# Kernel tuning notes

Hardware: AMD Instinct MI355X
Metric: run time of the kernel (lower is better)

Reference implementation:

```python
import jax, jax.numpy as jnp
import numpy as np

DIM = 192
HEADS = 4
EMBED = 48


def setup_inputs() -> dict:
    key = jax.random.key(0)
    ks = jax.random.split(key, 8)
    b, c, h, w = 8, DIM, 128, 128
    x = jax.random.normal(ks[0], (b, c, h, w), dtype=jnp.float32)
    prior = jax.random.normal(ks[1], (b, 1, EMBED * 4), dtype=jnp.float32)
    # learned params (bias=False)
    w_qkv = jax.random.normal(ks[2], (3 * c, c), dtype=jnp.float32) * (1.0 / np.sqrt(c))
    w_dw = jax.random.normal(ks[3], (3 * c, 1, 3, 3), dtype=jnp.float32) * (1.0 / 3.0)
    w_proj = jax.random.normal(ks[4], (c, c), dtype=jnp.float32) * (1.0 / np.sqrt(c))
    w_kernel = jax.random.normal(ks[5], (2 * c, EMBED * 4), dtype=jnp.float32) * (1.0 / np.sqrt(EMBED * 4))
    temperature = jnp.ones((HEADS, 1, 1), dtype=jnp.float32)
    return {"x": x, "prior": prior, "w_qkv": w_qkv, "w_dw": w_dw,
            "w_proj": w_proj, "w_kernel": w_kernel, "temperature": temperature}


def _mdta(x, prior, w_qkv, w_dw, w_proj, w_kernel, temperature):
    b, c, h, w = x.shape
    # prior modulation: Linear(4*embed -> 2*dim), broadcast over (h,w)
    kv = jnp.einsum('blf,of->blo', prior, w_kernel)[:, 0]        # (b, 2c)
    kv1, kv2 = kv[:, :c], kv[:, c:]
    x = x * kv1[:, :, None, None] + kv2[:, :, None, None]
    # 1x1 conv -> depthwise 3x3 conv
    qkv = jnp.einsum('bchw,oc->bohw', x, w_qkv)                   # (b, 3c, h, w)
    qkv = jax.lax.conv_general_dilated(
        qkv, w_dw, window_strides=(1, 1), padding='SAME',
        dimension_numbers=('NCHW', 'OIHW', 'NCHW'), feature_group_count=3 * c)
    q, k, v = jnp.split(qkv, 3, axis=1)
    ch = c // HEADS
    def heads(t):  # (b, c, h, w) -> (b, head, ch, h*w)
        return t.reshape(b, HEADS, ch, h * w)
    q, k, v = heads(q), heads(k), heads(v)
    # L2 normalize over the (h w) reduction axis
    q = q / jnp.linalg.norm(q, axis=-1, keepdims=True).clip(1e-12)
    k = k / jnp.linalg.norm(k, axis=-1, keepdims=True).clip(1e-12)
    attn = jnp.einsum('bhcn,bhdn->bhcd', q, k) * temperature      # (b, head, ch, ch)
    attn = jax.nn.softmax(attn, axis=-1)
    out = jnp.einsum('bhcd,bhdn->bhcn', attn, v).reshape(b, c, h, w)
    return jnp.einsum('bchw,oc->bohw', out, w_proj)


def reference(x, prior, w_qkv, w_dw, w_proj, w_kernel, temperature):
    return _mdta(x, prior, w_qkv, w_dw, w_proj, w_kernel, temperature)
```

## Files before the change

kernel.cpp:

```cpp
#include <hip/hip_runtime.h>
#include <hip/hip_bf16.h>
#include <stdint.h>

typedef float f32x4 __attribute__((ext_vector_type(4)));
typedef __bf16 bf16x8 __attribute__((ext_vector_type(8)));
typedef __bf16 bf16x4 __attribute__((ext_vector_type(4)));
typedef __bf16 bf16x2 __attribute__((ext_vector_type(2)));

#define NB 8
#define NC 192
#define NO 576
#define NH 128
#define NWID 128
#define NSP 16384
#define NHEADS 4
#define NCH 48

#define OFF_KV    0u
#define OFF_SSQ   12288u
#define OFF_S     24576u
#define OFF_WB    319488u
#define OFF_M     540672u
#define OFF_XT    1130496u
#define OFF_QKV1  152125440u

#define GR(r) (((r) ^ ((r) >> 2)) & 7)

__device__ __forceinline__ void g2l16(const void* g, void* l) {
    __builtin_amdgcn_global_load_lds((const __attribute__((address_space(1))) void*)g,
                                     (__attribute__((address_space(3))) void*)l, 16, 0, 0);
}

__global__ void k_prep(const float* __restrict__ prior, const float* __restrict__ w_kernel,
                       const float* __restrict__ w_qkv, float* __restrict__ kv,
                       float* __restrict__ zbase, __bf16* __restrict__ Wb) {
    int t = blockIdx.x * 256 + threadIdx.x;
    if (t < 76800) zbase[t] = 0.f;
    if (t < NO * NC) Wb[t] = (__bf16)w_qkv[t];
    if (t < NB * 384) {
        int b = t / 384, j = t % 384;
        const float* p = prior + b * NC;
        const float* wk = w_kernel + j * NC;
        float s = 0.f;
        for (int f = 0; f < NC; ++f) s += p[f] * wk[f];
        kv[t] = s;
    }
}

__global__ __launch_bounds__(256) void k_xt(const float* __restrict__ x, const float* __restrict__ kv,
                                            __bf16* __restrict__ xt) {
    int b = blockIdx.y;
    int n0 = blockIdx.x * 128;
    __shared__ __align__(16) __bf16 lds[128 * 192];
    int t = threadIdx.x;
    for (int p = 0; p < 24; ++p) {
        int id = p * 256 + t;
        int c = id >> 5, n4 = (id & 31) << 2;
        f32x4 v = *reinterpret_cast<const f32x4*>(x + (size_t)(b * NC + c) * NSP + n0 + n4);
        float k1 = kv[b * 384 + c], k2 = kv[b * 384 + 192 + c];
        int chi = (c >> 3) ^ ((n4 >> 2) & 7);
        int base = chi * 16 + (c & 7) * 2;
#pragma unroll
        for (int j = 0; j < 4; ++j)
            *reinterpret_cast<__bf16*>((char*)lds + (n4 + j) * 384 + base) = (__bf16)(v[j] * k1 + k2);
    }
    __syncthreads();
    for (int p = 0; p < 12; ++p) {
        int id = p * 256 + t;
        int n = id / 24, k = id % 24;
        bf16x8 r = *reinterpret_cast<const bf16x8*>((char*)lds + n * 384 + ((k ^ ((n >> 2) & 7)) << 4));
        *reinterpret_cast<bf16x8*>(xt + (size_t)(b * NSP + n0 + n) * NC + k * 8) = r;
    }
}

__global__ __launch_bounds__(256, 3) void k_qkv(const __bf16* __restrict__ xt, const __bf16* __restrict__ Wb,
                                                __bf16* __restrict__ qkv1) {
    __shared__ __align__(16) char lds[49152];
    int b = blockIdx.y, n0 = blockIdx.x * 64;
    int t = threadIdx.x;
    const __bf16* bsrc = xt + (size_t)(b * NSP + n0) * NC;
#pragma unroll
    for (int i = 0; i < 6; ++i) {
        int s = i * 256 + t;
        int r = s / 24, c = s % 24, g = c ^ (r & 7);
        g2l16(bsrc + (size_t)r * NC + g * 8, lds + s * 16);
    }
#pragma unroll
    for (int i = 0; i < 6; ++i) {
        int s = i * 256 + t;
        int r = s / 24, c = s % 24, g = c ^ (r & 7);
        g2l16(Wb + (size_t)r * NC + g * 8, lds + 24576 + s * 16);
    }
    asm volatile("s_waitcnt vmcnt(0)" ::: "memory");
    __syncthreads();
    int w = t >> 6, l = t & 63, lr = l & 15, lg = l >> 4;
    bf16x8 bgf[6];
#pragma unroll
    for (int ks = 0; ks < 6; ++ks) {
        int c16 = ks * 4 + lg;
        int r = w * 16 + lr;
        bgf[ks] = *reinterpret_cast<const bf16x8*>(lds + r * 384 + ((c16 ^ (r & 7)) << 4));
    }
    for (int ot = 0; ot < 9; ++ot) {
        f32x4 acc[4] = {};
#pragma unroll
        for (int ks = 0; ks < 6; ++ks) {
            int c16 = ks * 4 + lg;
            bf16x8 a[4];
#pragma unroll
            for (int mf = 0; mf < 4; ++mf) {
                int r = mf * 16 + lr;
                a[mf] = *reinterpret_cast<const bf16x8*>(lds + 24576 + r * 384 + ((c16 ^ (r & 7)) << 4));
            }
#pragma unroll
            for (int mf = 0; mf < 4; ++mf)
                acc[mf] = __builtin_amdgcn_mfma_f32_16x16x32_bf16(a[mf], bgf[ks], acc[mf], 0, 0, 0);
        }
        __syncthreads();
        if (ot < 8) {
            const __bf16* asrc = Wb + (size_t)(ot + 1) * 64 * NC;
#pragma unroll
            for (int i = 0; i < 6; ++i) {
                int s = i * 256 + t;
                int r = s / 24, c = s % 24, g = c ^ (r & 7);
                g2l16(asrc + (size_t)r * NC + g * 8, lds + 24576 + s * 16);
            }
            __builtin_amdgcn_sched_barrier(0);
        }
        int o0 = ot * 64;
#pragma unroll
        for (int mf = 0; mf < 4; ++mf)
#pragma unroll
            for (int rr = 0; rr < 4; ++rr) {
                int orow = o0 + mf * 16 + lg * 4 + rr;
                qkv1[(size_t)(b * NO + orow) * NSP + n0 + w * 16 + lr] = (__bf16)acc[mf][rr];
            }
        if (ot < 8) {
            asm volatile("s_waitcnt vmcnt(16)" ::: "memory");
            __syncthreads();
        }
    }
}

__global__ __launch_bounds__(256) void k_dw(const __bf16* __restrict__ qkv1, const float* __restrict__ w_dw,
                                            __bf16* __restrict__ qkv2, float* __restrict__ ssq) {
    int task = blockIdx.x * 4 + (threadIdx.x >> 6);
    int l = threadIdx.x & 63;
    int strip = task & 7;
    int bo = task >> 3;
    int o = bo % NO, b = bo / NO;
    const __bf16* src = qkv1 + (size_t)bo * NSP;
    __bf16* dst = qkv2 + (size_t)bo * NSP;
    float wd[9];
#pragma unroll
    for (int i = 0; i < 9; ++i) wd[i] = w_dw[o * 9 + i];
    int ys = strip * 16;
    float a0, b0, L0, R0, a1, b1, L1, R1, a2, b2, L2, R2;

#define LOADROW(Y, A, B, L_, R_) {                                            \
        bf16x2 p = {};                                                        \
        int y_ = (Y);                                                         \
        if (y_ >= 0 && y_ < NH) p = *reinterpret_cast<const bf16x2*>(src + y_ * NWID + 2 * l); \
        A = (float)p[0]; B = (float)p[1];                                     \
        L_ = __shfl(B, l - 1); R_ = __shfl(A, l + 1);                         \
        if (l == 0) L_ = 0.f;                                                 \
        if (l == 63) R_ = 0.f; }

    LOADROW(ys - 1, a0, b0, L0, R0)
    LOADROW(ys,     a1, b1, L1, R1)
    float ss = 0.f;
    bool qk = (o < 384);
#pragma unroll 4
    for (int i = 0; i < 16; ++i) {
        LOADROW(ys + i + 1, a2, b2, L2, R2)
        float oa = L0 * wd[0] + a0 * wd[1] + b0 * wd[2]
                 + L1 * wd[3] + a1 * wd[4] + b1 * wd[5]
                 + L2 * wd[6] + a2 * wd[7] + b2 * wd[8];
        float ob = a0 * wd[0] + b0 * wd[1] + R0 * wd[2]
                 + a1 * wd[3] + b1 * wd[4] + R1 * wd[5]
                 + a2 * wd[6] + b2 * wd[7] + R2 * wd[8];
        bf16x2 ov; ov[0] = (__bf16)oa; ov[1] = (__bf16)ob;
        *reinterpret_cast<bf16x2*>(dst + (ys + i) * NWID + 2 * l) = ov;
        if (qk) { float fa = (float)ov[0], fb = (float)ov[1]; ss += fa * fa + fb * fb; }
        a0 = a1; b0 = b1; L0 = L1; R0 = R1;
        a1 = a2; b1 = b2; L1 = L2; R1 = R2;
    }
#undef LOADROW
    if (qk) {
        for (int off = 32; off > 0; off >>= 1) ss += __shfl_down(ss, off);
        if (l == 0) atomicAdd(&ssq[b * 384 + o], ss);
    }
}

__global__ __launch_bounds__(256, 3) void k_sdot(const __bf16* __restrict__ qkv2, float* __restrict__ S) {
    __shared__ __align__(16) char lds[49152];
    int b = blockIdx.z, h = blockIdx.y, n0 = blockIdx.x * 512;
    int t = threadIdx.x;
    int w = t >> 6, l = t & 63, lr = l & 15, lg = l >> 4;
    const __bf16* qsrc = qkv2 + (size_t)(b * NO + h * NCH) * NSP + n0;
    const __bf16* ksrc = qkv2 + (size_t)(b * NO + 192 + h * NCH) * NSP + n0;
    f32x4 acc[3][3] = {};
    for (int pass = 0; pass < 2; ++pass) {
        if (pass) __syncthreads();
        int coff = pass * 256;
#pragma unroll
        for (int i = 0; i < 6; ++i) {
            int s = i * 256 + t;
            int r = s >> 5, c = s & 31, g = c ^ (r & 7);
            g2l16(qsrc + (size_t)r * NSP + coff + g * 8, lds + s * 16);
        }
#pragma unroll
        for (int i = 0; i < 6; ++i) {
            int s = i * 256 + t;
            int r = s >> 5, c = s & 31, g = c ^ (r & 7);
            g2l16(ksrc + (size_t)r * NSP + coff + g * 8, lds + 24576 + s * 16);
        }
        asm volatile("s_waitcnt vmcnt(0)" ::: "memory");
        __syncthreads();
#pragma unroll
        for (int j = 0; j < 2; ++j) {
            int c16 = (w * 2 + j) * 4 + lg;
            bf16x8 a[3], bb[3];
#pragma unroll
            for (int mf = 0; mf < 3; ++mf) {
                int r = mf * 16 + lr;
                a[mf] = *reinterpret_cast<const bf16x8*>(lds + r * 512 + ((c16 ^ (r & 7)) << 4));
            }
#pragma unroll
            for (int nf = 0; nf < 3; ++nf) {
                int r = nf * 16 + lr;
                bb[nf] = *reinterpret_cast<const bf16x8*>(lds + 24576 + r * 512 + ((c16 ^ (r & 7)) << 4));
            }
#pragma unroll
            for (int mf = 0; mf < 3; ++mf)
#pragma unroll
                for (int nf = 0; nf < 3; ++nf)
                    acc[mf][nf] = __builtin_amdgcn_mfma_f32_16x16x32_bf16(a[mf], bb[nf], acc[mf][nf], 0, 0, 0);
        }
    }
    __syncthreads();
    float* red = (float*)lds;
#pragma unroll
    for (int mf = 0; mf < 3; ++mf)
#pragma unroll
        for (int nf = 0; nf < 3; ++nf)
#pragma unroll
            for (int r = 0; r < 4; ++r) {
                int c = mf * 16 + lg * 4 + r, d = nf * 16 + lr;
                red[(w * 48 + c) * 49 + d] = acc[mf][nf][r];
            }
    __syncthreads();
    float* Sb = S + (size_t)(b * NHEADS + h) * NCH * NCH;
    for (int i = 0; i < 9; ++i) {
        int idx = t + i * 256;
        int c = idx / 48, d = idx % 48;
        float s = red[c * 49 + d] + red[(48 + c) * 49 + d] + red[(96 + c) * 49 + d] + red[(144 + c) * 49 + d];
        atomicAdd(&Sb[c * 48 + d], s);
    }
}

__global__ __launch_bounds__(256) void k_soft(const float* __restrict__ S, const float* __restrict__ ssq,
                                              const float* __restrict__ temp, const float* __restrict__ w_proj,
                                              __bf16* __restrict__ M) {
    int b = blockIdx.x / NHEADS, h = blockIdx.x % NHEADS;
    int tid = threadIdx.x;
    __shared__ float attn[48][48];
    __shared__ float inv[96];
    if (tid < 96) {
        int c = tid % 48;
        int isK = tid / 48;
        float v = ssq[b * 384 + isK * 192 + h * NCH + c];
        float nrm = fmaxf(sqrtf(v), 1e-12f);
        inv[tid] = 1.f / nrm;
    }
    __syncthreads();
    float tp = temp[h];
    const float* Sb = S + (size_t)(b * NHEADS + h) * NCH * NCH;
    for (int i = 0; i < 9; ++i) {
        int idx = tid + i * 256;
        int c = idx / 48, d = idx % 48;
        attn[c][d] = Sb[c * 48 + d] * inv[c] * inv[48 + d] * tp;
    }
    __syncthreads();
    if (tid < 48) {
        float m = -1e30f;
        for (int d = 0; d < 48; ++d) m = fmaxf(m, attn[tid][d]);
        float sum = 0.f;
        for (int d = 0; d < 48; ++d) { float e = __expf(attn[tid][d] - m); attn[tid][d] = e; sum += e; }
        float r = 1.f / sum;
        for (int d = 0; d < 48; ++d) attn[tid][d] *= r;
    }
    __syncthreads();
    for (int i = 0; i < 36; ++i) {
        int idx = tid + i * 256;
        int oo = idx / 48, d = idx % 48;
        const float* wp = w_proj + oo * NC + h * NCH;
        float s = 0.f;
        for (int c = 0; c < 48; ++c) s += wp[c] * attn[c][d];
        M[(size_t)(b * NC + oo) * NC + h * NCH + d] = (__bf16)s;
    }
}

__global__ __launch_bounds__(256, 2) void k_out(const __bf16* __restrict__ Mw, const __bf16* __restrict__ qkv2,
                                                float* __restrict__ outp) {
    __shared__ __align__(16) char lds[73728];
    int b = blockIdx.y, n0 = blockIdx.x * 128;
    int t = threadIdx.x;
    const __bf16* asrc0 = Mw + (size_t)(b * NC) * NC;
#pragma unroll
    for (int i = 0; i < 6; ++i) {
        int s = i * 256 + t;
        int r = s / 24, c = s % 24, g = c ^ GR(r);
        g2l16(asrc0 + (size_t)r * NC + g * 8, lds + 49152 + s * 16);
    }
    const __bf16* vb = qkv2 + (size_t)(b * NO + 384) * NSP + n0;
#pragma unroll 4
    for (int p = 0; p < 24; ++p) {
        int id = p * 256 + t;
        int c = id >> 5, n4 = (id & 31) << 2;
        bf16x4 vv = *reinterpret_cast<const bf16x4*>(vb + (size_t)c * NSP + n4);
#pragma unroll
        for (int j = 0; j < 4; ++j) {
            int n = n4 + j;
            int chi = (c >> 3) ^ GR(n);
            *reinterpret_cast<__bf16*>((char*)lds + n * 384 + chi * 16 + (c & 7) * 2) = vv[j];
        }
    }
    asm volatile("s_waitcnt vmcnt(0)" ::: "memory");
    __syncthreads();
    int w = t >> 6, l = t & 63, lr = l & 15, lg = l >> 4;
    bf16x8 bgf[6][2];
#pragma unroll
    for (int ks = 0; ks < 6; ++ks) {
        int c16 = ks * 4 + lg;
#pragma unroll
        for (int nf = 0; nf < 2; ++nf) {
            int r = w * 32 + nf * 16 + lr;
            bgf[ks][nf] = *reinterpret_cast<const bf16x8*>(lds + r * 384 + ((c16 ^ GR(r)) << 4));
        }
    }
    for (int ot = 0; ot < 3; ++ot) {
        f32x4 acc[4][2] = {};
#pragma unroll
        for (int ks = 0; ks < 6; ++ks) {
            int c16 = ks * 4 + lg;
            bf16x8 a[4];
#pragma unroll
            for (int mf = 0; mf < 4; ++mf) {
                int r = mf * 16 + lr;
                a[mf] = *reinterpret_cast<const bf16x8*>(lds + 49152 + r * 384 + ((c16 ^ GR(r)) << 4));
            }
#pragma unroll
            for (int mf = 0; mf < 4; ++mf)
#pragma unroll
                for (int nf = 0; nf < 2; ++nf)
                    acc[mf][nf] = __builtin_amdgcn_mfma_f32_16x16x32_bf16(a[mf], bgf[ks][nf], acc[mf][nf], 0, 0, 0);
        }
        __syncthreads();
        if (ot < 2) {
            const __bf16* asrc = Mw + (size_t)(b * NC + (ot + 1) * 64) * NC;
#pragma unroll
            for (int i = 0; i < 6; ++i) {
                int s = i * 256 + t;
                int r = s / 24, c = s % 24, g = c ^ GR(r);
                g2l16(asrc + (size_t)r * NC + g * 8, lds + 49152 + s * 16);
            }
            __builtin_amdgcn_sched_barrier(0);
        }
        int o0 = ot * 64;
#pragma unroll
        for (int mf = 0; mf < 4; ++mf)
#pragma unroll
            for (int rr = 0; rr < 4; ++rr) {
                int orow = o0 + mf * 16 + lg * 4 + rr;
#pragma unroll
                for (int nf = 0; nf < 2; ++nf)
                    outp[(size_t)(b * NC + orow) * NSP + n0 + w * 32 + nf * 16 + lr] = acc[mf][nf][rr];
            }
        if (ot < 2) {
            asm volatile("s_waitcnt vmcnt(32)" ::: "memory");
            __syncthreads();
        }
    }
}

extern "C" void kernel_launch(void* const* d_in, const int* in_sizes, int n_in,
                              void* d_out, int out_size, void* d_ws, size_t ws_size,
                              hipStream_t stream) {
    const float* x        = (const float*)d_in[0];
    const float* prior    = (const float*)d_in[1];
    const float* w_qkv    = (const float*)d_in[2];
    const float* w_dw     = (const float*)d_in[3];
    const float* w_proj   = (const float*)d_in[4];
    const float* w_kernel = (const float*)d_in[5];
    const float* temp     = (const float*)d_in[6];
    char* ws = (char*)d_ws;
    float*  kv    = (float*)(ws + OFF_KV);
    float*  ssq   = (float*)(ws + OFF_SSQ);
    float*  S     = (float*)(ws + OFF_S);
    __bf16* Wb    = (__bf16*)(ws + OFF_WB);
    __bf16* M     = (__bf16*)(ws + OFF_M);
    __bf16* xt    = (__bf16*)(ws + OFF_XT);
    __bf16* qkv2  = (__bf16*)(ws + OFF_XT);
    __bf16* qkv1  = (__bf16*)(ws + OFF_QKV1);
    float*  outp  = (float*)d_out;

    k_prep<<<432, 256, 0, stream>>>(prior, w_kernel, w_qkv, kv, (float*)(ws + OFF_SSQ), Wb);
    k_xt<<<dim3(128, 8), 256, 0, stream>>>(x, kv, xt);
    k_qkv<<<dim3(256, 8), 256, 0, stream>>>(xt, Wb, qkv1);
    k_dw<<<9216, 256, 0, stream>>>(qkv1, w_dw, qkv2, ssq);
    k_sdot<<<dim3(32, 4, 8), 256, 0, stream>>>(qkv2, S);
    k_soft<<<32, 256, 0, stream>>>(S, ssq, temp, w_proj, M);
    k_out<<<dim3(128, 8), 256, 0, stream>>>(M, qkv2, outp);
}
```

Before: 227.9 us.

## Restructure qkv GEMM to keep weight tile in registers and stream activations

The 1x1-conv GEMM kernel now assigns each block one 64-row output tile and a 1024-column spatial range. The weight fragments for that tile are held in registers, and each wave streams its own 16-column activation slices through double-buffered LDS using async global-to-LDS loads. This removes per-tile block-wide barriers and the reloading of weight tiles into LDS, and it overlaps the activation loads with MFMA work. In exchange the activation matrix is read nine times (once per output tile), register pressure rises from 24 bf16x8 fragments, and the grid becomes 16x9x8. The depthwise LOADROW macro is also moved to file scope with an explicit source argument.

```diff
diff --git a/kernel.cpp b/kernel.cpp
--- a/kernel.cpp
+++ b/kernel.cpp
@@ -30,6 +30,15 @@
     __builtin_amdgcn_global_load_lds((const __attribute__((address_space(1))) void*)g,
                                      (__attribute__((address_space(3))) void*)l, 16, 0, 0);
 }
+
+#define LOADROW(SRC, Y, A, B, L_, R_) {                                       \
+        bf16x2 p = {};                                                        \
+        int y_ = (Y);                                                         \
+        if (y_ >= 0 && y_ < NH) p = *reinterpret_cast<const bf16x2*>((SRC) + y_ * NWID + 2 * l); \
+        A = (float)p[0]; B = (float)p[1];                                     \
+        L_ = __shfl(B, l - 1); R_ = __shfl(A, l + 1);                         \
+        if (l == 0) L_ = 0.f;                                                 \
+        if (l == 63) R_ = 0.f; }
 
 __global__ void k_prep(const float* __restrict__ prior, const float* __restrict__ w_kernel,
                        const float* __restrict__ w_qkv, float* __restrict__ kv,
@@ -76,69 +85,56 @@
 __global__ __launch_bounds__(256, 3) void k_qkv(const __bf16* __restrict__ xt, const __bf16* __restrict__ Wb,
                                                 __bf16* __restrict__ qkv1) {
     __shared__ __align__(16) char lds[49152];
-    int b = blockIdx.y, n0 = blockIdx.x * 64;
-    int t = threadIdx.x;
-    const __bf16* bsrc = xt + (size_t)(b * NSP + n0) * NC;
-#pragma unroll
-    for (int i = 0; i < 6; ++i) {
-        int s = i * 256 + t;
+    int b = blockIdx.z, ot = blockIdx.y;
+    int nbase = blockIdx.x * 1024;
+    int t = threadIdx.x, w = t >> 6, l = t & 63, lr = l & 15, lg = l >> 4;
+    char* wlds = lds + w * 12288;
+    const __bf16* bsrc0 = xt + (size_t)(b * NSP + nbase + w * 16) * NC;
+#pragma unroll
+    for (int j = 0; j < 6; ++j) {
+        int s = j * 64 + l;
         int r = s / 24, c = s % 24, g = c ^ (r & 7);
-        g2l16(bsrc + (size_t)r * NC + g * 8, lds + s * 16);
-    }
-#pragma unroll
-    for (int i = 0; i < 6; ++i) {
-        int s = i * 256 + t;
-        int r = s / 24, c = s % 24, g = c ^ (r & 7);
-        g2l16(Wb + (size_t)r * NC + g * 8, lds + 24576 + s * 16);
-    }
-    asm volatile("s_waitcnt vmcnt(0)" ::: "memory");
-    __syncthreads();
-    int w = t >> 6, l = t & 63, lr = l & 15, lg = l >> 4;
-    bf16x8 bgf[6];
-#pragma unroll
-    for (int ks = 0; ks < 6; ++ks) {
-        int c16 = ks * 4 + lg;
-        int r = w * 16 + lr;
-        bgf[ks] = *reinterpret_cast<const bf16x8*>(lds + r * 384 + ((c16 ^ (r & 7)) << 4));
-    }
-    for (int ot = 0; ot < 9; ++ot) {
+        g2l16(bsrc0 + (size_t)r * NC + g * 8, wlds + s * 16);
+    }
+    const __bf16* asrc = Wb + (size_t)(ot * 64 + lr) * NC + lg * 8;
+    bf16x8 ag[4][6];
+#pragma unroll
+    for (int mf = 0; mf < 4; ++mf)
+#pragma unroll
+        for (int ks = 0; ks < 6; ++ks)
+            ag[mf][ks] = *reinterpret_cast<const bf16x8*>(asrc + (size_t)mf * 16 * NC + ks * 32);
+    for (int i = 0; i < 16; ++i) {
+        int cur = i & 1;
+        if (i < 15) {
+            const __bf16* bsrc = xt + (size_t)(b * NSP + nbase + (i + 1) * 64 + w * 16) * NC;
+#pragma unroll
+            for (int j = 0; j < 6; ++j) {
+                int s = j * 64 + l;
+                int r = s / 24, c = s % 24, g = c ^ (r & 7);
+                g2l16(bsrc + (size_t)r * NC + g * 8, wlds + (cur ^ 1) * 6144 + s * 16);
+            }
+            __builtin_amdgcn_sched_barrier(0);
+        }
+        if (i == 0)      asm volatile("s_waitcnt vmcnt(30)" ::: "memory");
+        else if (i < 15) asm volatile("s_waitcnt vmcnt(22)" ::: "memory");
+        else             asm volatile("s_waitcnt vmcnt(16)" ::: "memory");
         f32x4 acc[4] = {};
 #pragma unroll
         for (int ks = 0; ks < 6; ++ks) {
-            int c16 = ks * 4 + lg;
-            bf16x8 a[4];
-#pragma unroll
-            for (int mf = 0; mf < 4; ++mf) {
-                int r = mf * 16 + lr;
-                a[mf] = *reinterpret_cast<const bf16x8*>(lds + 24576 + r * 384 + ((c16 ^ (r & 7)) << 4));
-            }
+            bf16x8 bg = *reinterpret_cast<const bf16x8*>(
+                wlds + cur * 6144 + lr * 384 + (((ks * 4 + lg) ^ (lr & 7)) << 4));
 #pragma unroll
             for (int mf = 0; mf < 4; ++mf)
-                acc[mf] = __builtin_amdgcn_mfma_f32_16x16x32_bf16(a[mf], bgf[ks], acc[mf], 0, 0, 0);
-        }
-        __syncthreads();
-        if (ot < 8) {
-            const __bf16* asrc = Wb + (size_t)(ot + 1) * 64 * NC;
-#pragma unroll
-            for (int i = 0; i < 6; ++i) {
-                int s = i * 256 + t;
-                int r = s / 24, c = s % 24, g = c ^ (r & 7);
-                g2l16(asrc + (size_t)r * NC + g * 8, lds + 24576 + s * 16);
-            }
-            __builtin_amdgcn_sched_barrier(0);
-        }
-        int o0 = ot * 64;
+                acc[mf] = __builtin_amdgcn_mfma_f32_16x16x32_bf16(ag[mf][ks], bg, acc[mf], 0, 0, 0);
+        }
+        int n = nbase + i * 64 + w * 16 + lr;
 #pragma unroll
         for (int mf = 0; mf < 4; ++mf)
 #pragma unroll
             for (int rr = 0; rr < 4; ++rr) {
-                int orow = o0 + mf * 16 + lg * 4 + rr;
-                qkv1[(size_t)(b * NO + orow) * NSP + n0 + w * 16 + lr] = (__bf16)acc[mf][rr];
-            }
-        if (ot < 8) {
-            asm volatile("s_waitcnt vmcnt(16)" ::: "memory");
-            __syncthreads();
-        }
+                int orow = ot * 64 + mf * 16 + lg * 4 + rr;
+                qkv1[(size_t)(b * NO + orow) * NSP + n] = (__bf16)acc[mf][rr];
+            }
     }
 }
 
@@ -156,23 +152,13 @@
     for (int i = 0; i < 9; ++i) wd[i] = w_dw[o * 9 + i];
     int ys = strip * 16;
     float a0, b0, L0, R0, a1, b1, L1, R1, a2, b2, L2, R2;
-
-#define LOADROW(Y, A, B, L_, R_) {                                            \
-        bf16x2 p = {};                                                        \
-        int y_ = (Y);                                                         \
-        if (y_ >= 0 && y_ < NH) p = *reinterpret_cast<const bf16x2*>(src + y_ * NWID + 2 * l); \
-        A = (float)p[0]; B = (float)p[1];                                     \
-        L_ = __shfl(B, l - 1); R_ = __shfl(A, l + 1);                         \
-        if (l == 0) L_ = 0.f;                                                 \
-        if (l == 63) R_ = 0.f; }
-
-    LOADROW(ys - 1, a0, b0, L0, R0)
-    LOADROW(ys,     a1, b1, L1, R1)
+    LOADROW(src, ys - 1, a0, b0, L0, R0)
+    LOADROW(src, ys,     a1, b1, L1, R1)
     float ss = 0.f;
     bool qk = (o < 384);
 #pragma unroll 4
     for (int i = 0; i < 16; ++i) {
-        LOADROW(ys + i + 1, a2, b2, L2, R2)
+        LOADROW(src, ys + i + 1, a2, b2, L2, R2)
         float oa = L0 * wd[0] + a0 * wd[1] + b0 * wd[2]
                  + L1 * wd[3] + a1 * wd[4] + b1 * wd[5]
                  + L2 * wd[6] + a2 * wd[7] + b2 * wd[8];
@@ -185,7 +171,6 @@
         a0 = a1; b0 = b1; L0 = L1; R0 = R1;
         a1 = a2; b1 = b2; L1 = L2; R1 = R2;
     }
-#undef LOADROW
     if (qk) {
         for (int off = 32; off > 0; off >>= 1) ss += __shfl_down(ss, off);
         if (l == 0) atomicAdd(&ssq[b * 384 + o], ss);
@@ -407,7 +392,7 @@
 
     k_prep<<<432, 256, 0, stream>>>(prior, w_kernel, w_qkv, kv, (float*)(ws + OFF_SSQ), Wb);
     k_xt<<<dim3(128, 8), 256, 0, stream>>>(x, kv, xt);
-    k_qkv<<<dim3(256, 8), 256, 0, stream>>>(xt, Wb, qkv1);
+    k_qkv<<<dim3(16, 9, 8), 256, 0, stream>>>(xt, Wb, qkv1);
     k_dw<<<9216, 256, 0, stream>>>(qkv1, w_dw, qkv2, ssq);
     k_sdot<<<dim3(32, 4, 8), 256, 0, stream>>>(qkv2, S);
     k_soft<<<32, 256, 0, stream>>>(S, ssq, temp, w_proj, M);
```

New measurement: 315.6 us. 38.5% more time.
